# Optimization experiments

Measured on AMD Instinct MI355X. Metric: run time of the kernel, lower is better.

Reference implementation:

```python
import jax, jax.numpy as jnp
import numpy as np

N = 100000   # vertices
E = 600000   # directed edges
F = 200000   # triangle faces
CIN = 128
COUT = 128
H = 32       # metric MLP hidden
D = 3        # embedding_dim (3D metric)
TRI = D * (D + 1) // 2  # 6 params of a symmetric 3x3


def setup_inputs() -> dict:
    key = jax.random.key(0)
    ks = jax.random.split(key, 8)
    features = jax.random.normal(ks[0], (N, CIN), jnp.float32)
    vertices = jax.random.normal(ks[1], (N, 3), jnp.float32)
    edges = jax.random.randint(ks[2], (2, E), 0, N)
    faces = jax.random.randint(ks[3], (3, F), 0, N)
    # metric MLP params (edge tangent vector -> symmetric metric params)
    W1 = jax.random.normal(ks[4], (D, H), jnp.float32) / np.sqrt(D)
    b1 = jnp.zeros((H,), jnp.float32)
    W2 = jax.random.normal(ks[5], (H, TRI), jnp.float32) / np.sqrt(H)
    b2 = jnp.zeros((TRI,), jnp.float32)
    # per-vertex feature transform
    Wlin = jax.random.normal(ks[6], (CIN, COUT), jnp.float32) / np.sqrt(CIN)
    blin = jnp.zeros((COUT,), jnp.float32)
    return dict(features=features, vertices=vertices, edges=edges, faces=faces,
                W1=W1, b1=b1, W2=W2, b2=b2, Wlin=Wlin, blin=blin)


def _vertex_normals(vertices, faces):
    # area-weighted vertex normals from triangle faces
    v0, v1, v2 = vertices[faces[0]], vertices[faces[1]], vertices[faces[2]]
    fn = jnp.cross(v1 - v0, v2 - v0)                       # [F,3]
    n = jnp.zeros_like(vertices)
    n = n.at[faces[0]].add(fn).at[faces[1]].add(fn).at[faces[2]].add(fn)
    return n / (jnp.linalg.norm(n, axis=-1, keepdims=True) + 1e-8)


def _sym_from_flat(theta):
    # theta [E,6] -> symmetric [E,3,3]
    iu0, iu1 = jnp.triu_indices(D)
    S = jnp.zeros((theta.shape[0], D, D), theta.dtype)
    S = S.at[:, iu0, iu1].set(theta)
    S = S.at[:, iu1, iu0].set(theta)
    return S


def reference(features, vertices, edges, faces, W1, b1, W2, b2, Wlin, blin):
    eps = 1e-5
    src, dst = edges[0], edges[1]
    normals = _vertex_normals(vertices, faces)             # [N,3] ('tangent' info)
    d = vertices[dst] - vertices[src]                      # [E,3] edge vectors
    n_src = normals[src]
    t = d - jnp.sum(d * n_src, -1, keepdims=True) * n_src  # tangent-plane projection
    # learned metric per edge: MLP -> symmetric S, PSD metric M = S S
    h = jax.nn.relu(t @ W1 + b1)                           # [E,H]
    theta = h @ W2 + b2                                    # [E,6]
    S = _sym_from_flat(theta)                              # [E,3,3]
    M = jnp.einsum('eij,ejk->eik', S, S)                   # PSD metric
    q = jnp.einsum('ei,eij,ej->e', t, M, t)                # metric quadratic form
    w = jnp.exp(-q)                                        # positive edge weights
    # per-vertex linear, then metric-weighted mean aggregation over in-edges
    x = features @ Wlin + blin                             # [N,COUT]
    num = jax.ops.segment_sum(w[:, None] * x[src], dst, num_segments=N)
    den = jax.ops.segment_sum(w, dst, num_segments=N) + eps
    out = num / den[:, None]                               # MetricConv output
    # MetricConvBlock: manual per-feature normalization + ELU
    mu = out.mean(axis=0)
    sd = out.std(axis=0, ddof=1)                           # torch std is unbiased
    out = (out - mu) / (sd + eps)
    return jax.nn.elu(out)
```

## Files before the change

### kernel.cpp

```cpp
#include <hip/hip_runtime.h>
#include <hip/hip_bf16.h>
#include <math.h>

#define N_V 100000
#define N_E 600000
#define N_F 200000

typedef __attribute__((ext_vector_type(8))) short bf16x8;
typedef __attribute__((ext_vector_type(4))) float f32x4;

#define FUSED_BLOCKS 1563
#define FACE_BLOCKS 782
#define EDGE_BLOCKS 2344
#define PACK_BLOCKS 64

__device__ __forceinline__ unsigned short f2bf(float f) {
    unsigned int u = __builtin_bit_cast(unsigned int, f);
    u += 0x7fffu + ((u >> 16) & 1u);
    return (unsigned short)(u >> 16);
}

__global__ void k_fn(const float* __restrict__ vtx, const int* __restrict__ faces,
                     const float* __restrict__ Wlin,
                     float* __restrict__ fnbuf,
                     int* __restrict__ head_f, int* __restrict__ next_f,
                     unsigned short* __restrict__ Wb) {
    int b = blockIdx.x;
    int t = threadIdx.x;
    if (b < FACE_BLOCKS) {
        int f = b * 256 + t;
        if (f >= N_F) return;
        int i0 = faces[f], i1 = faces[N_F + f], i2 = faces[2 * N_F + f];
        #pragma unroll
        for (int j = 0; j < 3; j++) {
            int v = (j == 0) ? i0 : (j == 1 ? i1 : i2);
            int c = 3 * f + j;
            int old = atomicExch(&head_f[v], c);
            next_f[c] = old;
        }
        float ax = vtx[3 * i0], ay = vtx[3 * i0 + 1], az = vtx[3 * i0 + 2];
        float bx = vtx[3 * i1] - ax, by = vtx[3 * i1 + 1] - ay, bz = vtx[3 * i1 + 2] - az;
        float cx = vtx[3 * i2] - ax, cy = vtx[3 * i2 + 1] - ay, cz = vtx[3 * i2 + 2] - az;
        fnbuf[f]           = by * cz - bz * cy;
        fnbuf[N_F + f]     = bz * cx - bx * cz;
        fnbuf[2 * N_F + f] = bx * cy - by * cx;
    } else {
        int i = (b - FACE_BLOCKS) * 256 + t;
        int j = i & 7;
        int lane = (i >> 3) & 63;
        int ct = (i >> 9) & 7;
        int kk = i >> 12;
        int k = kk * 32 + (lane >> 4) * 8 + j;
        int n = ct * 16 + (lane & 15);
        Wb[i] = f2bf(Wlin[k * 128 + n]);
    }
}

__global__ void k_vnorm(const float* __restrict__ fnbuf,
                        const int* __restrict__ head_f, const int* __restrict__ next_f,
                        float* __restrict__ nrm) {
    int v = blockIdx.x * 256 + threadIdx.x;
    if (v >= N_V) return;
    float nx = 0.f, ny = 0.f, nz = 0.f;
    int c = head_f[v];
    while (c >= 0) {
        int f = (unsigned)c / 3u;
        nx += fnbuf[f];
        ny += fnbuf[N_F + f];
        nz += fnbuf[2 * N_F + f];
        c = next_f[c];
    }
    float inv = 1.f / (sqrtf(nx * nx + ny * ny + nz * nz) + 1e-8f);
    nrm[3 * v] = nx * inv; nrm[3 * v + 1] = ny * inv; nrm[3 * v + 2] = nz * inv;
}

__global__ void k_edge(const float* __restrict__ vtx, const int* __restrict__ edges,
                       const float* __restrict__ nrm,
                       const float* __restrict__ W1, const float* __restrict__ b1,
                       const float* __restrict__ W2, const float* __restrict__ b2,
                       float* __restrict__ wbuf,
                       int* __restrict__ head_e, int* __restrict__ next_e) {
    __shared__ float sW1[96], sb1[32], sW2[192], sb2[6];
    int t = threadIdx.x;
    if (t < 96)  sW1[t] = W1[t];
    if (t < 32)  sb1[t] = b1[t];
    if (t < 192) sW2[t] = W2[t];
    if (t < 6)   sb2[t] = b2[t];
    __syncthreads();
    int e = blockIdx.x * blockDim.x + t;
    if (e >= N_E) return;
    int s = edges[e], d = edges[N_E + e];
    int old = atomicExch(&head_e[d], e);
    float dx = vtx[3 * d] - vtx[3 * s];
    float dy = vtx[3 * d + 1] - vtx[3 * s + 1];
    float dz = vtx[3 * d + 2] - vtx[3 * s + 2];
    float nx = nrm[3 * s], ny = nrm[3 * s + 1], nz = nrm[3 * s + 2];
    float dp = dx * nx + dy * ny + dz * nz;
    float tx = dx - dp * nx, ty = dy - dp * ny, tz = dz - dp * nz;
    float th0 = sb2[0], th1 = sb2[1], th2 = sb2[2], th3 = sb2[3], th4 = sb2[4], th5 = sb2[5];
    #pragma unroll
    for (int j = 0; j < 32; j++) {
        float h = tx * sW1[j] + ty * sW1[32 + j] + tz * sW1[64 + j] + sb1[j];
        h = fmaxf(h, 0.f);
        const float* w2r = &sW2[j * 6];
        th0 += h * w2r[0]; th1 += h * w2r[1]; th2 += h * w2r[2];
        th3 += h * w2r[3]; th4 += h * w2r[4]; th5 += h * w2r[5];
    }
    float ux = th0 * tx + th1 * ty + th2 * tz;
    float uy = th1 * tx + th3 * ty + th4 * tz;
    float uz = th2 * tx + th4 * ty + th5 * tz;
    float q = ux * ux + uy * uy + uz * uz;
    next_e[e] = old;
    wbuf[e] = expf(-q);
}

__global__ __launch_bounds__(512) void k_fused(const float* __restrict__ feat,
                                               const int* __restrict__ edges,
                                               const int* __restrict__ head_e,
                                               const int* __restrict__ next_e,
                                               const float* __restrict__ wbuf,
                                               const unsigned short* __restrict__ Wb,
                                               const float* __restrict__ blin,
                                               float* __restrict__ out,
                                               float* __restrict__ partials) {
    __shared__ __align__(16) unsigned short At[64 * 136];
    __shared__ float gs[64];
    int t = threadIdx.x;
    int hw = t >> 5;
    int hl = t & 31;

    #pragma unroll
    for (int rep = 0; rep < 4; rep++) {
        int row = rep * 16 + hw;
        int v = blockIdx.x * 64 + row;
        float4 acc = {0.f, 0.f, 0.f, 0.f};
        float den = 0.f;
        if (v < N_V) {
            int e = head_e[v];
            while (e >= 0) {
                int s = edges[e];
                float w = wbuf[e];
                float4 f = *(const float4*)(feat + (size_t)s * 128 + 4 * hl);
                acc.x += w * f.x; acc.y += w * f.y; acc.z += w * f.z; acc.w += w * f.w;
                den += w;
                e = next_e[e];
            }
        }
        float inv = 1.f / (den + 1e-5f);
        ushort4 p;
        p.x = f2bf(acc.x * inv); p.y = f2bf(acc.y * inv);
        p.z = f2bf(acc.z * inv); p.w = f2bf(acc.w * inv);
        *(ushort4*)(&At[row * 136 + 4 * hl]) = p;
        if (hl == 0) gs[row] = den * inv;
    }
    __syncthreads();

    int ct = t >> 6;
    int lane = t & 63;
    int m = lane & 15, quad = lane >> 4;
    bf16x8 bfr[4];
    #pragma unroll
    for (int kk = 0; kk < 4; kk++)
        bfr[kk] = *(const bf16x8*)(Wb + (((kk * 8 + ct) * 64 + lane) << 3));
    float bl = blin[ct * 16 + m];
    float ssr = 0.f, qqr = 0.f;
    #pragma unroll
    for (int tile = 0; tile < 4; tile++) {
        f32x4 acc = (f32x4){0.f, 0.f, 0.f, 0.f};
        #pragma unroll
        for (int kk = 0; kk < 4; kk++) {
            bf16x8 af = *(const bf16x8*)(&At[(tile * 16 + m) * 136 + kk * 32 + quad * 8]);
            acc = __builtin_amdgcn_mfma_f32_16x16x32_bf16(af, bfr[kk], acc, 0, 0, 0);
        }
        int r0 = blockIdx.x * 64 + tile * 16;
        #pragma unroll
        for (int reg = 0; reg < 4; reg++) {
            int r = r0 + quad * 4 + reg;
            float g = gs[tile * 16 + quad * 4 + reg];
            float val = acc[reg] + bl * g;
            if (r < N_V) out[(size_t)r * 128 + ct * 16 + m] = val;
            ssr += val; qqr += val * val;
        }
    }
    ssr += __shfl_xor(ssr, 16); qqr += __shfl_xor(qqr, 16);
    ssr += __shfl_xor(ssr, 32); qqr += __shfl_xor(qqr, 32);
    if (quad == 0) {
        partials[(size_t)blockIdx.x * 256 + ct * 16 + m] = ssr;
        partials[(size_t)blockIdx.x * 256 + 128 + ct * 16 + m] = qqr;
    }
}

__global__ __launch_bounds__(64) void k_rstats(const float* __restrict__ partials,
                                               float* __restrict__ stats) {
    int c = blockIdx.x;
    int lane = threadIdx.x;
    float s = 0.f, q = 0.f;
    for (int b = lane; b < FUSED_BLOCKS; b += 64) {
        s += partials[(size_t)b * 256 + c];
        q += partials[(size_t)b * 256 + 128 + c];
    }
    #pragma unroll
    for (int off = 32; off; off >>= 1) {
        s += __shfl_down(s, off);
        q += __shfl_down(q, off);
    }
    if (lane == 0) {
        float mu = s * (1.f / N_V);
        float var = (q - s * mu) * (1.f / (N_V - 1));
        float sd = sqrtf(fmaxf(var, 0.f));
        stats[c] = mu;
        stats[128 + c] = 1.f / (sd + 1e-5f);
    }
}

__global__ void k_finalize(float* __restrict__ out, const float* __restrict__ stats) {
    int i = blockIdx.x * blockDim.x + threadIdx.x;
    if (i >= N_V * 32) return;
    float4 v = ((float4*)out)[i];
    int c0 = (i * 4) & 127;
    float mu0 = stats[c0], mu1 = stats[c0 + 1], mu2 = stats[c0 + 2], mu3 = stats[c0 + 3];
    float is0 = stats[128 + c0], is1 = stats[128 + c0 + 1], is2 = stats[128 + c0 + 2], is3 = stats[128 + c0 + 3];
    v.x = (v.x - mu0) * is0; v.y = (v.y - mu1) * is1;
    v.z = (v.z - mu2) * is2; v.w = (v.w - mu3) * is3;
    v.x = v.x > 0.f ? v.x : expm1f(v.x);
    v.y = v.y > 0.f ? v.y : expm1f(v.y);
    v.z = v.z > 0.f ? v.z : expm1f(v.z);
    v.w = v.w > 0.f ? v.w : expm1f(v.w);
    ((float4*)out)[i] = v;
}

extern "C" void kernel_launch(void* const* d_in, const int* in_sizes, int n_in,
                              void* d_out, int out_size, void* d_ws, size_t ws_size,
                              hipStream_t stream) {
    const float* feat  = (const float*)d_in[0];
    const float* vtx   = (const float*)d_in[1];
    const int*   edges = (const int*)d_in[2];
    const int*   faces = (const int*)d_in[3];
    const float* W1   = (const float*)d_in[4];
    const float* b1   = (const float*)d_in[5];
    const float* W2   = (const float*)d_in[6];
    const float* b2   = (const float*)d_in[7];
    const float* Wlin = (const float*)d_in[8];
    const float* blin = (const float*)d_in[9];
    float* out = (float*)d_out;

    float* ws = (float*)d_ws;
    int*   head_e   = (int*)ws;
    int*   head_f   = (int*)(ws + 100000);
    float* nrm      = ws + 200000;
    float* partials = ws + 100000;
    float* fnbuf    = ws + 500128;
    int*   next_e   = (int*)(ws + 500128);
    int*   next_f   = (int*)(ws + 1100128);
    float* wbuf     = ws + 1100128;
    unsigned short* Wb = (unsigned short*)(ws + 1700128);
    float* stats    = ws;

    hipMemsetAsync(d_ws, 0xFF, 200000 * sizeof(int), stream);

    k_fn<<<FACE_BLOCKS + PACK_BLOCKS, 256, 0, stream>>>(vtx, faces, Wlin, fnbuf,
                                                        head_f, next_f, Wb);
    k_vnorm<<<(N_V + 255) / 256, 256, 0, stream>>>(fnbuf, head_f, next_f, nrm);
    k_edge<<<EDGE_BLOCKS, 256, 0, stream>>>(vtx, edges, nrm, W1, b1, W2, b2,
                                            wbuf, head_e, next_e);
    k_fused<<<FUSED_BLOCKS, 512, 0, stream>>>(feat, edges, head_e, next_e, wbuf,
                                              Wb, blin, out, partials);
    k_rstats<<<128, 64, 0, stream>>>(partials, stats);
    k_finalize<<<(N_V * 32 + 255) / 256, 256, 0, stream>>>(out, stats);
}
```

Baseline: 289.6 us.

## Pack edge list nodes and interleave four vertex chains in aggregation

Each edge's next pointer, source index and bf16 edge weight are packed into one 8-byte node, so the gather loop does one dependent load per hop instead of three. Each half-warp now walks four vertices' linked lists at the same time instead of one after another, which keeps more independent memory requests in flight. Face normals are stored as float4 so the vertex-normal loop does one vector load, and the workspace layout and memsets are rearranged to match. The cost is that edge weights are rounded to bf16 before aggregation, and the packing relies on index bit widths (20-bit next pointer, 17-bit source index) that only fit these problem sizes.

```diff
diff --git a/kernel.cpp b/kernel.cpp
--- a/kernel.cpp
+++ b/kernel.cpp
@@ -22,7 +22,7 @@
 
 __global__ void k_fn(const float* __restrict__ vtx, const int* __restrict__ faces,
                      const float* __restrict__ Wlin,
-                     float* __restrict__ fnbuf,
+                     float4* __restrict__ fnbuf4,
                      int* __restrict__ head_f, int* __restrict__ next_f,
                      unsigned short* __restrict__ Wb) {
     int b = blockIdx.x;
@@ -41,9 +41,12 @@
         float ax = vtx[3 * i0], ay = vtx[3 * i0 + 1], az = vtx[3 * i0 + 2];
         float bx = vtx[3 * i1] - ax, by = vtx[3 * i1 + 1] - ay, bz = vtx[3 * i1 + 2] - az;
         float cx = vtx[3 * i2] - ax, cy = vtx[3 * i2 + 1] - ay, cz = vtx[3 * i2 + 2] - az;
-        fnbuf[f]           = by * cz - bz * cy;
-        fnbuf[N_F + f]     = bz * cx - bx * cz;
-        fnbuf[2 * N_F + f] = bx * cy - by * cx;
+        float4 fn;
+        fn.x = by * cz - bz * cy;
+        fn.y = bz * cx - bx * cz;
+        fn.z = bx * cy - by * cx;
+        fn.w = 0.f;
+        fnbuf4[f] = fn;
     } else {
         int i = (b - FACE_BLOCKS) * 256 + t;
         int j = i & 7;
@@ -56,7 +59,7 @@
     }
 }
 
-__global__ void k_vnorm(const float* __restrict__ fnbuf,
+__global__ void k_vnorm(const float4* __restrict__ fnbuf4,
                         const int* __restrict__ head_f, const int* __restrict__ next_f,
                         float* __restrict__ nrm) {
     int v = blockIdx.x * 256 + threadIdx.x;
@@ -64,10 +67,8 @@
     float nx = 0.f, ny = 0.f, nz = 0.f;
     int c = head_f[v];
     while (c >= 0) {
-        int f = (unsigned)c / 3u;
-        nx += fnbuf[f];
-        ny += fnbuf[N_F + f];
-        nz += fnbuf[2 * N_F + f];
+        float4 fn = fnbuf4[(unsigned)c / 3u];
+        nx += fn.x; ny += fn.y; nz += fn.z;
         c = next_f[c];
     }
     float inv = 1.f / (sqrtf(nx * nx + ny * ny + nz * nz) + 1e-8f);
@@ -78,8 +79,7 @@
                        const float* __restrict__ nrm,
                        const float* __restrict__ W1, const float* __restrict__ b1,
                        const float* __restrict__ W2, const float* __restrict__ b2,
-                       float* __restrict__ wbuf,
-                       int* __restrict__ head_e, int* __restrict__ next_e) {
+                       int* __restrict__ head_e, uint2* __restrict__ enode) {
     __shared__ float sW1[96], sb1[32], sW2[192], sb2[6];
     int t = threadIdx.x;
     if (t < 96)  sW1[t] = W1[t];
@@ -110,15 +110,17 @@
     float uy = th1 * tx + th3 * ty + th4 * tz;
     float uz = th2 * tx + th4 * ty + th5 * tz;
     float q = ux * ux + uy * uy + uz * uz;
-    next_e[e] = old;
-    wbuf[e] = expf(-q);
+    float w = expf(-q);
+    unsigned int w16 = f2bf(w);
+    uint2 nd;
+    nd.x = (unsigned int)(old + 1) | ((w16 & 0xFFFu) << 20);
+    nd.y = (unsigned int)s | ((w16 >> 12) << 17);
+    enode[e] = nd;
 }
 
 __global__ __launch_bounds__(512) void k_fused(const float* __restrict__ feat,
-                                               const int* __restrict__ edges,
                                                const int* __restrict__ head_e,
-                                               const int* __restrict__ next_e,
-                                               const float* __restrict__ wbuf,
+                                               const uint2* __restrict__ enode,
                                                const unsigned short* __restrict__ Wb,
                                                const float* __restrict__ blin,
                                                float* __restrict__ out,
@@ -128,30 +130,64 @@
     int t = threadIdx.x;
     int hw = t >> 5;
     int hl = t & 31;
-
-    #pragma unroll
-    for (int rep = 0; rep < 4; rep++) {
-        int row = rep * 16 + hw;
-        int v = blockIdx.x * 64 + row;
-        float4 acc = {0.f, 0.f, 0.f, 0.f};
-        float den = 0.f;
-        if (v < N_V) {
-            int e = head_e[v];
-            while (e >= 0) {
-                int s = edges[e];
-                float w = wbuf[e];
-                float4 f = *(const float4*)(feat + (size_t)s * 128 + 4 * hl);
-                acc.x += w * f.x; acc.y += w * f.y; acc.z += w * f.z; acc.w += w * f.w;
-                den += w;
-                e = next_e[e];
-            }
-        }
-        float inv = 1.f / (den + 1e-5f);
+    int vb = blockIdx.x * 64 + hw * 4;
+
+    float4 a0 = {0,0,0,0}, a1 = {0,0,0,0}, a2 = {0,0,0,0}, a3 = {0,0,0,0};
+    float d0 = 0.f, d1 = 0.f, d2 = 0.f, d3 = 0.f;
+    int e0 = (vb + 0 < N_V) ? head_e[vb + 0] : -1;
+    int e1 = (vb + 1 < N_V) ? head_e[vb + 1] : -1;
+    int e2 = (vb + 2 < N_V) ? head_e[vb + 2] : -1;
+    int e3 = (vb + 3 < N_V) ? head_e[vb + 3] : -1;
+
+    while ((e0 >= 0) || (e1 >= 0) || (e2 >= 0) || (e3 >= 0)) {
+        if (e0 >= 0) {
+            uint2 nd = enode[e0];
+            unsigned int wb = (nd.x >> 20) | (((nd.y >> 17) & 0xFu) << 12);
+            float w = __builtin_bit_cast(float, wb << 16);
+            const float4 f = *(const float4*)(feat + (size_t)(nd.y & 0x1FFFFu) * 128 + 4 * hl);
+            a0.x += w * f.x; a0.y += w * f.y; a0.z += w * f.z; a0.w += w * f.w;
+            d0 += w;
+            e0 = (int)(nd.x & 0xFFFFFu) - 1;
+        }
+        if (e1 >= 0) {
+            uint2 nd = enode[e1];
+            unsigned int wb = (nd.x >> 20) | (((nd.y >> 17) & 0xFu) << 12);
+            float w = __builtin_bit_cast(float, wb << 16);
+            const float4 f = *(const float4*)(feat + (size_t)(nd.y & 0x1FFFFu) * 128 + 4 * hl);
+            a1.x += w * f.x; a1.y += w * f.y; a1.z += w * f.z; a1.w += w * f.w;
+            d1 += w;
+            e1 = (int)(nd.x & 0xFFFFFu) - 1;
+        }
+        if (e2 >= 0) {
+            uint2 nd = enode[e2];
+            unsigned int wb = (nd.x >> 20) | (((nd.y >> 17) & 0xFu) << 12);
+            float w = __builtin_bit_cast(float, wb << 16);
+            const float4 f = *(const float4*)(feat + (size_t)(nd.y & 0x1FFFFu) * 128 + 4 * hl);
+            a2.x += w * f.x; a2.y += w * f.y; a2.z += w * f.z; a2.w += w * f.w;
+            d2 += w;
+            e2 = (int)(nd.x & 0xFFFFFu) - 1;
+        }
+        if (e3 >= 0) {
+            uint2 nd = enode[e3];
+            unsigned int wb = (nd.x >> 20) | (((nd.y >> 17) & 0xFu) << 12);
+            float w = __builtin_bit_cast(float, wb << 16);
+            const float4 f = *(const float4*)(feat + (size_t)(nd.y & 0x1FFFFu) * 128 + 4 * hl);
+            a3.x += w * f.x; a3.y += w * f.y; a3.z += w * f.z; a3.w += w * f.w;
+            d3 += w;
+            e3 = (int)(nd.x & 0xFFFFFu) - 1;
+        }
+    }
+    #pragma unroll
+    for (int j = 0; j < 4; j++) {
+        float4 a = (j == 0) ? a0 : (j == 1) ? a1 : (j == 2) ? a2 : a3;
+        float dn = (j == 0) ? d0 : (j == 1) ? d1 : (j == 2) ? d2 : d3;
+        float inv = 1.f / (dn + 1e-5f);
         ushort4 p;
-        p.x = f2bf(acc.x * inv); p.y = f2bf(acc.y * inv);
-        p.z = f2bf(acc.z * inv); p.w = f2bf(acc.w * inv);
+        p.x = f2bf(a.x * inv); p.y = f2bf(a.y * inv);
+        p.z = f2bf(a.z * inv); p.w = f2bf(a.w * inv);
+        int row = hw * 4 + j;
         *(ushort4*)(&At[row * 136 + 4 * hl]) = p;
-        if (hl == 0) gs[row] = den * inv;
+        if (hl == 0) gs[row] = dn * inv;
     }
     __syncthreads();
 
@@ -246,25 +282,25 @@
 
     float* ws = (float*)d_ws;
     int*   head_e   = (int*)ws;
-    int*   head_f   = (int*)(ws + 100000);
-    float* nrm      = ws + 200000;
+    float* nrm3     = ws + 100000;
     float* partials = ws + 100000;
-    float* fnbuf    = ws + 500128;
-    int*   next_e   = (int*)(ws + 500128);
-    int*   next_f   = (int*)(ws + 1100128);
-    float* wbuf     = ws + 1100128;
-    unsigned short* Wb = (unsigned short*)(ws + 1700128);
+    int*   head_f   = (int*)(ws + 500128);
+    int*   next_f   = (int*)(ws + 600128);
+    float4* fnbuf4  = (float4*)(ws + 1200128);
+    uint2* enode    = (uint2*)(ws + 500128);
+    unsigned short* Wb = (unsigned short*)(ws + 2000128);
     float* stats    = ws;
 
-    hipMemsetAsync(d_ws, 0xFF, 200000 * sizeof(int), stream);
-
-    k_fn<<<FACE_BLOCKS + PACK_BLOCKS, 256, 0, stream>>>(vtx, faces, Wlin, fnbuf,
+    hipMemsetAsync(head_e, 0xFF, 100000 * sizeof(int), stream);
+    hipMemsetAsync(head_f, 0xFF, 100000 * sizeof(int), stream);
+
+    k_fn<<<FACE_BLOCKS + PACK_BLOCKS, 256, 0, stream>>>(vtx, faces, Wlin, fnbuf4,
                                                         head_f, next_f, Wb);
-    k_vnorm<<<(N_V + 255) / 256, 256, 0, stream>>>(fnbuf, head_f, next_f, nrm);
-    k_edge<<<EDGE_BLOCKS, 256, 0, stream>>>(vtx, edges, nrm, W1, b1, W2, b2,
-                                            wbuf, head_e, next_e);
-    k_fused<<<FUSED_BLOCKS, 512, 0, stream>>>(feat, edges, head_e, next_e, wbuf,
-                                              Wb, blin, out, partials);
+    k_vnorm<<<(N_V + 255) / 256, 256, 0, stream>>>(fnbuf4, head_f, next_f, nrm3);
+    k_edge<<<EDGE_BLOCKS, 256, 0, stream>>>(vtx, edges, nrm3, W1, b1, W2, b2,
+                                            head_e, enode);
+    k_fused<<<FUSED_BLOCKS, 512, 0, stream>>>(feat, head_e, enode, Wb, blin,
+                                              out, partials);
     k_rstats<<<128, 64, 0, stream>>>(partials, stats);
     k_finalize<<<(N_V * 32 + 255) / 256, 256, 0, stream>>>(out, stats);
 }
```

Result: faster. 280.2 us (-3.2%).
